# Kernel optimization log

Hardware: AMD Instinct MI355X
Metric: run time of the kernel (lower is better)

## Reference

```python
import jax, jax.numpy as jnp
import numpy as np

N_NODES = 50000
N_EDGES = 800000
F_EXP = 128
F_CNV = 64
HID = 128
N_CLASSES = 10
N_GRAPHS = 64
SLOPE = 0.2


def setup_inputs() -> dict:
    key = jax.random.key(0)
    ks = jax.random.split(key, 24)
    inp = {
        "exp": jax.random.normal(ks[0], (N_NODES, F_EXP), dtype=jnp.float32),
        "cnv": jax.random.normal(ks[1], (N_NODES, F_CNV), dtype=jnp.float32),
        "edge_index": jax.random.randint(ks[2], (2, N_EDGES), 0, N_NODES, dtype=jnp.int64 if jax.config.jax_enable_x64 else jnp.int32),
        "batch": jnp.sort(jax.random.randint(ks[3], (N_NODES,), 0, N_GRAPHS)),
    }
    s = 0.02
    def lin(k, fi, fo):
        kw, kb = jax.random.split(k)
        return (jax.random.normal(kw, (fi, fo), jnp.float32) * s,
                jax.random.normal(kb, (fo,), jnp.float32) * s)
    inp["eps1e"] = jnp.zeros((), jnp.float32)
    inp["W1e"], inp["b1e"] = lin(ks[4], F_EXP, HID)
    inp["eps2e"] = jnp.zeros((), jnp.float32)
    inp["W2e"], inp["b2e"] = lin(ks[5], HID, HID)
    inp["eps1c"] = jnp.zeros((), jnp.float32)
    inp["W1c"], inp["b1c"] = lin(ks[6], F_CNV, HID)
    inp["eps2c"] = jnp.zeros((), jnp.float32)
    inp["W2c"], inp["b2c"] = lin(ks[7], HID, HID)
    inp["Wm"], inp["bm"] = lin(ks[8], 2 * HID, HID)
    inp["Wp1"], inp["bp1"] = lin(ks[9], HID, HID)
    inp["Wp2"], inp["bp2"] = lin(ks[10], HID, N_CLASSES)
    return inp


def _lrelu(x):
    return jnp.where(x > 0, x, SLOPE * x)


def _forward(exp, cnv, src, dst, batch,
             eps1e, W1e, b1e, eps2e, W2e, b2e,
             eps1c, W1c, b1c, eps2c, W2c, b2c,
             Wm, bm, Wp1, bp1, Wp2, bp2):
    N = exp.shape[0]

    def gin(x, eps, W, b):
        # scatter-add neighbor aggregation over edges (self-loops included in src/dst)
        agg = jax.ops.segment_sum(x[src], dst, num_segments=N)
        return ((1.0 + eps) * x + agg) @ W + b

    x_exp = _lrelu(gin(exp, eps1e, W1e, b1e))
    x_exp = _lrelu(gin(x_exp, eps2e, W2e, b2e))
    x_cnv = _lrelu(gin(cnv, eps1c, W1c, b1c))
    x_cnv = _lrelu(gin(x_cnv, eps2c, W2c, b2c))
    x = jnp.concatenate([x_exp, x_cnv], axis=1) @ Wm + bm
    x = _lrelu(x)

    # global mean pool over graph ids
    counts = jax.ops.segment_sum(jnp.ones((N,), x.dtype), batch, num_segments=N_GRAPHS)
    counts = jnp.maximum(counts, 1.0)[:, None]
    graph_repr = jax.ops.segment_sum(x, batch, num_segments=N_GRAPHS) / counts

    logits_nodes = _lrelu(x @ Wp1 + bp1)  # nn.ReLU in mlp -> actually ReLU
    logits_nodes = jnp.maximum(x @ Wp1 + bp1, 0.0) @ Wp2 + bp2
    graph_logits = jax.ops.segment_sum(logits_nodes, batch, num_segments=N_GRAPHS) / counts
    return graph_repr, graph_logits


def reference(exp, cnv, edge_index, batch,
              eps1e, W1e, b1e, eps2e, W2e, b2e,
              eps1c, W1c, b1c, eps2c, W2c, b2c,
              Wm, bm, Wp1, bp1, Wp2, bp2):
    N = exp.shape[0]
    loop = jnp.arange(N, dtype=edge_index.dtype)
    src = jnp.concatenate([edge_index[0], loop])
    dst = jnp.concatenate([edge_index[1], loop])
    return _forward(exp, cnv, src, dst, batch,
                    eps1e, W1e, b1e, eps2e, W2e, b2e,
                    eps1c, W1c, b1c, eps2c, W2c, b2c,
                    Wm, bm, Wp1, bp1, Wp2, bp2)
```

## Files before the change

### kernel.cpp

```cpp
#include <hip/hip_runtime.h>

#define N_NODES 50000
#define N_PAD   50016
#define N_EDGES 800000
#define HID 128
#define NCLS 10
#define NG 64
#define PWAVE 32
#define NB_SCAN ((N_NODES + 255) / 256)

#define EPART 8
#define PRANGE ((N_NODES + EPART - 1) / EPART)
#define ECHUNK 4096
#define NCHUNK ((N_EDGES + ECHUNK - 1) / ECHUNK)

typedef unsigned int uint32;
typedef __attribute__((ext_vector_type(8))) short bf16x8;
typedef __attribute__((ext_vector_type(4))) float f32x4;

__device__ __forceinline__ unsigned short f2bf(float f) {
    uint32 u = __float_as_uint(f);
    uint32 r = u + 0x7fffu + ((u >> 16) & 1u);
    return (unsigned short)(r >> 16);
}
__device__ __forceinline__ float bflo(uint32 v) { return __uint_as_float(v << 16); }
__device__ __forceinline__ float bfhi(uint32 v) { return __uint_as_float(v & 0xffff0000u); }
__device__ __forceinline__ uint32 packbf(float a, float b) {
    return (uint32)f2bf(a) | ((uint32)f2bf(b) << 16);
}


__global__ __launch_bounds__(256) void count_part_k(const int* __restrict__ dst,
                                                    int* __restrict__ deg) {
    int part = blockIdx.x & 7;
    int chunk = blockIdx.x >> 3;
    int lo = part * PRANGE;
    int hi = min(lo + PRANGE, N_NODES);
    int e0 = chunk * ECHUNK;
    int e1 = min(e0 + ECHUNK, N_EDGES);
    for (int i = e0 + threadIdx.x; i < e1; i += 256) {
        int d = dst[i];
        if (d >= lo && d < hi) atomicAdd(&deg[d], 1);
    }
}

__global__ __launch_bounds__(256) void scatter_part_k(const int* __restrict__ src,
                                                      const int* __restrict__ dst,
                                                      int* __restrict__ cursor,
                                                      int* __restrict__ csr) {
    int part = blockIdx.x & 7;
    int chunk = blockIdx.x >> 3;
    int lo = part * PRANGE;
    int hi = min(lo + PRANGE, N_NODES);
    int e0 = chunk * ECHUNK;
    int e1 = min(e0 + ECHUNK, N_EDGES);
    for (int i = e0 + threadIdx.x; i < e1; i += 256) {
        int d = dst[i];
        if (d >= lo && d < hi) {
            int pos = atomicAdd(&cursor[d], 1);
            csr[pos] = src[i];
        }
    }
}

__global__ void gbounds_k(const int* __restrict__ batch, int* __restrict__ gstart) {
    int i = blockIdx.x * blockDim.x + threadIdx.x;
    if (i >= N_NODES) return;
    int b = batch[i];
    int prev = (i == 0) ? -1 : batch[i - 1];
    for (int g = prev + 1; g <= b; g++) gstart[g] = i;
    if (i == N_NODES - 1) {
        for (int g = b + 1; g <= NG; g++) gstart[g] = N_NODES;
    }
}

__device__ __forceinline__ int block_excl_scan_256(int v, int tid, int* total_out) {
    int lane = tid & 63, w = tid >> 6;
    int x = v;
#pragma unroll
    for (int off = 1; off < 64; off <<= 1) {
        int y = __shfl_up(x, off, 64);
        if (lane >= off) x += y;
    }
    __shared__ int wsum[4];
    if (lane == 63) wsum[w] = x;
    __syncthreads();
    int add = 0;
#pragma unroll
    for (int i = 0; i < 4; i++) add += (i < w) ? wsum[i] : 0;
    int total = wsum[0] + wsum[1] + wsum[2] + wsum[3];
    if (total_out) *total_out = total;
    return x - v + add;
}

__global__ __launch_bounds__(256) void scan_partial_k(const int* __restrict__ deg,
                                                      int* __restrict__ rowptr,
                                                      int* __restrict__ blocksum) {
    int tid = threadIdx.x;
    int gid = blockIdx.x * 256 + tid;
    int v = (gid < N_NODES) ? deg[gid] : 0;
    int total;
    int excl = block_excl_scan_256(v, tid, &total);
    if (gid < N_NODES) rowptr[gid] = excl;
    if (tid == 0) blocksum[blockIdx.x] = total;
}

__global__ __launch_bounds__(256) void scan_root_k(const int* __restrict__ blocksum,
                                                   int* __restrict__ blockoff,
                                                   const int* __restrict__ gstart,
                                                   float* __restrict__ invcnt) {
    int tid = threadIdx.x;
    int v = (tid < NB_SCAN) ? blocksum[tid] : 0;
    int excl = block_excl_scan_256(v, tid, nullptr);
    if (tid < NB_SCAN) blockoff[tid] = excl;
    if (tid < NG) {
        int c = gstart[tid + 1] - gstart[tid];
        invcnt[tid] = (c > 0) ? 1.0f / (float)c : 0.0f;
    }
}

__global__ __launch_bounds__(256) void scan_add_k(int* __restrict__ rowptr,
                                                  int* __restrict__ cursor,
                                                  const int* __restrict__ blockoff) {
    int gid = blockIdx.x * 256 + threadIdx.x;
    if (gid < N_NODES) {
        int r = rowptr[gid] + blockoff[blockIdx.x];
        rowptr[gid] = r;
        cursor[gid] = r;
    }
    if (gid == 0) rowptr[N_NODES] = N_EDGES;
}


__global__ __launch_bounds__(256) void conv_both_k(const float* __restrict__ inE,
                                                   unsigned short* __restrict__ outE, int n4e,
                                                   const float* __restrict__ inC,
                                                   unsigned short* __restrict__ outC, int n4c) {
    int i = blockIdx.x * 256 + threadIdx.x;
    const float* in;
    unsigned short* out;
    if (i < n4e) { in = inE; out = outE; }
    else { i -= n4e; if (i >= n4c) return; in = inC; out = outC; }
    float4 v = *(const float4*)(in + (size_t)i * 4);
    uint2 o = {packbf(v.x, v.y), packbf(v.z, v.w)};
    *(uint2*)(out + (size_t)i * 4) = o;
}

__global__ __launch_bounds__(256) void wconv_all_k(const float* W1e, const float* W2e,
                                                   const float* W1c, const float* W2c,
                                                   const float* Wm, const float* Wp1,
                                                   unsigned short* WT1e, unsigned short* WT2e,
                                                   unsigned short* WT1c, unsigned short* WT2c,
                                                   unsigned short* WTm1, unsigned short* WTm2,
                                                   unsigned short* WTp1) {
    int b = blockIdx.x;
    int t = threadIdx.x;
    const float* W; unsigned short* WT; int i; int K;
    if (b < 64)       { W = W1e; WT = WT1e; i = b * 256 + t;          K = 128; }
    else if (b < 128) { W = W2e; WT = WT2e; i = (b - 64) * 256 + t;   K = 128; }
    else if (b < 160) { W = W1c; WT = WT1c; i = (b - 128) * 256 + t;  K = 64;  }
    else if (b < 224) { W = W2c; WT = WT2c; i = (b - 160) * 256 + t;  K = 128; }
    else if (b < 352) {
        i = (b - 224) * 256 + t;
        int k = i >> 7, n = i & 127;
        unsigned short v = f2bf(Wm[i]);
        if (k < 128) WTm1[n * 128 + k] = v;
        else         WTm2[n * 128 + (k - 128)] = v;
        return;
    }
    else              { W = Wp1; WT = WTp1; i = (b - 352) * 256 + t;  K = 128; }
    int k = i >> 7, n = i & 127;
    if (k < K) WT[n * K + k] = f2bf(W[i]);
}


__device__ __forceinline__ uint32 agg_row128(const uint32* __restrict__ X,
                                             const int* __restrict__ rowptr,
                                             const int* __restrict__ csr,
                                             int n, int lane, float scale) {
    uint32 xv = X[(size_t)n * 64 + lane];
    float a0 = scale * bflo(xv);
    float a1 = scale * bfhi(xv);
    int e = rowptr[n], e1 = rowptr[n + 1];
    for (; e + 8 <= e1; e += 8) {
        int i0 = csr[e],     i1 = csr[e + 1], i2 = csr[e + 2], i3 = csr[e + 3];
        int i4 = csr[e + 4], i5 = csr[e + 5], i6 = csr[e + 6], i7 = csr[e + 7];
        uint32 v0 = X[(size_t)i0 * 64 + lane];
        uint32 v1 = X[(size_t)i1 * 64 + lane];
        uint32 v2 = X[(size_t)i2 * 64 + lane];
        uint32 v3 = X[(size_t)i3 * 64 + lane];
        uint32 v4 = X[(size_t)i4 * 64 + lane];
        uint32 v5 = X[(size_t)i5 * 64 + lane];
        uint32 v6 = X[(size_t)i6 * 64 + lane];
        uint32 v7 = X[(size_t)i7 * 64 + lane];
        a0 += bflo(v0) + bflo(v1) + bflo(v2) + bflo(v3) +
              bflo(v4) + bflo(v5) + bflo(v6) + bflo(v7);
        a1 += bfhi(v0) + bfhi(v1) + bfhi(v2) + bfhi(v3) +
              bfhi(v4) + bfhi(v5) + bfhi(v6) + bfhi(v7);
    }
    if (e + 4 <= e1) {
        int i0 = csr[e], i1 = csr[e + 1], i2 = csr[e + 2], i3 = csr[e + 3];
        uint32 v0 = X[(size_t)i0 * 64 + lane];
        uint32 v1 = X[(size_t)i1 * 64 + lane];
        uint32 v2 = X[(size_t)i2 * 64 + lane];
        uint32 v3 = X[(size_t)i3 * 64 + lane];
        a0 += bflo(v0) + bflo(v1) + bflo(v2) + bflo(v3);
        a1 += bfhi(v0) + bfhi(v1) + bfhi(v2) + bfhi(v3);
        e += 4;
    }
    for (; e < e1; e++) {
        uint32 v = X[(size_t)csr[e] * 64 + lane];
        a0 += bflo(v);
        a1 += bfhi(v);
    }
    return packbf(a0, a1);
}


__global__ __launch_bounds__(256) void agg_gemm_k(const uint32* __restrict__ X1,
                                                  const float* __restrict__ eps1,
                                                  const unsigned short* __restrict__ WT1p,
                                                  const float* __restrict__ b1,
                                                  unsigned short* __restrict__ out1,
                                                  const uint32* __restrict__ X2,
                                                  const float* __restrict__ eps2,
                                                  const unsigned short* __restrict__ WT2p,
                                                  const float* __restrict__ b2,
                                                  unsigned short* __restrict__ out2,
                                                  const int* __restrict__ rowptr,
                                                  const int* __restrict__ csr,
                                                  int nblk1) {
    __shared__ uint32 lds[32 * 64];
    int blk = blockIdx.x;
    const uint32* X; const float* epsp; const unsigned short* WT;
    const float* bias; unsigned short* out;
    if (blk < nblk1) { X = X1; epsp = eps1; WT = WT1p; bias = b1; out = out1; }
    else { blk -= nblk1; X = X2; epsp = eps2; WT = WT2p; bias = b2; out = out2; }

    int tid = threadIdx.x;
    int w = tid >> 6, lane = tid & 63;
    int base = blk * 32;
    float scale = 2.0f + epsp[0];

    for (int s = 0; s < 8; s++) {
        int lrow = w * 8 + s;
        int n = base + lrow;
        uint32 outv = 0;
        if (n < N_NODES) outv = agg_row128(X, rowptr, csr, n, lane, scale);
        int byte = (lrow * 256 + lane * 4) ^ ((lrow & 7) << 4);
        lds[byte >> 2] = outv;
    }
    __syncthreads();

    int m = lane & 15, g = lane >> 4;
    int lrow = (w & 1) * 16 + m;
    int row16 = base + (w & 1) * 16;
    int col16 = (w >> 1) * 64;

    f32x4 acc[4];
#pragma unroll
    for (int nt = 0; nt < 4; nt++) acc[nt] = (f32x4){0.f, 0.f, 0.f, 0.f};

    const unsigned short* bp = WT + (size_t)(col16 + m) * 128 + g * 8;
#pragma unroll
    for (int k0 = 0; k0 < 128; k0 += 32) {
        int ab = (lrow * 256 + (g * 8 + k0) * 2) ^ ((lrow & 7) << 4);
        bf16x8 af = *(const bf16x8*)((const char*)lds + ab);
#pragma unroll
        for (int nt = 0; nt < 4; nt++) {
            bf16x8 bfv = *(const bf16x8*)(bp + (size_t)nt * 16 * 128 + k0);
            acc[nt] = __builtin_amdgcn_mfma_f32_16x16x32_bf16(af, bfv, acc[nt], 0, 0, 0);
        }
    }

#pragma unroll
    for (int nt = 0; nt < 4; nt++) {
        int col = col16 + nt * 16 + m;
        float bv = bias[col];
#pragma unroll
        for (int r = 0; r < 4; r++) {
            int row = row16 + g * 4 + r;
            if (row < N_NODES) {
                float v = acc[nt][r] + bv;
                v = v > 0.f ? v : 0.2f * v;
                out[(size_t)row * 128 + col] = f2bf(v);
            }
        }
    }
}


__global__ __launch_bounds__(256) void agg64_bf_k(const uint32* __restrict__ X,
                                                  const int* __restrict__ rowptr,
                                                  const int* __restrict__ csr,
                                                  const float* __restrict__ eps,
                                                  uint32* __restrict__ H) {
    int hw = (blockIdx.x * 256 + threadIdx.x) >> 5;
    int lane = threadIdx.x & 31;
    if (hw >= N_NODES) return;
    float scale = 2.0f + eps[0];
    uint32 xv = X[(size_t)hw * 32 + lane];
    float a0 = scale * bflo(xv);
    float a1 = scale * bfhi(xv);
    int e = rowptr[hw], e1 = rowptr[hw + 1];
    for (; e + 8 <= e1; e += 8) {
        int i0 = csr[e],     i1 = csr[e + 1], i2 = csr[e + 2], i3 = csr[e + 3];
        int i4 = csr[e + 4], i5 = csr[e + 5], i6 = csr[e + 6], i7 = csr[e + 7];
        uint32 v0 = X[(size_t)i0 * 32 + lane];
        uint32 v1 = X[(size_t)i1 * 32 + lane];
        uint32 v2 = X[(size_t)i2 * 32 + lane];
        uint32 v3 = X[(size_t)i3 * 32 + lane];
        uint32 v4 = X[(size_t)i4 * 32 + lane];
        uint32 v5 = X[(size_t)i5 * 32 + lane];
        uint32 v6 = X[(size_t)i6 * 32 + lane];
        uint32 v7 = X[(size_t)i7 * 32 + lane];
        a0 += bflo(v0) + bflo(v1) + bflo(v2) + bflo(v3) +
              bflo(v4) + bflo(v5) + bflo(v6) + bflo(v7);
        a1 += bfhi(v0) + bfhi(v1) + bfhi(v2) + bfhi(v3) +
              bfhi(v4) + bfhi(v5) + bfhi(v6) + bfhi(v7);
    }
    if (e + 4 <= e1) {
        int i0 = csr[e], i1 = csr[e + 1], i2 = csr[e + 2], i3 = csr[e + 3];
        uint32 v0 = X[(size_t)i0 * 32 + lane];
        uint32 v1 = X[(size_t)i1 * 32 + lane];
        uint32 v2 = X[(size_t)i2 * 32 + lane];
        uint32 v3 = X[(size_t)i3 * 32 + lane];
        a0 += bflo(v0) + bflo(v1) + bflo(v2) + bflo(v3);
        a1 += bfhi(v0) + bfhi(v1) + bfhi(v2) + bfhi(v3);
        e += 4;
    }
    for (; e < e1; e++) {
        uint32 v = X[(size_t)csr[e] * 32 + lane];
        a0 += bflo(v);
        a1 += bfhi(v);
    }
    H[(size_t)hw * 32 + lane] = packbf(a0, a1);
}


__global__ __launch_bounds__(256) void gemm_bf_k(const unsigned short* __restrict__ A1,
                                                 const unsigned short* __restrict__ WT1, int K1,
                                                 const unsigned short* __restrict__ A2,
                                                 const unsigned short* __restrict__ WT2, int K2,
                                                 const float* __restrict__ bias,
                                                 unsigned short* __restrict__ out, int act) {
    int tid = threadIdx.x;
    int w = tid >> 6, l = tid & 63;
    int row16 = blockIdx.x * 32 + (w & 1) * 16;
    int col16 = (w >> 1) * 64;
    int m = l & 15, g = l >> 4;

    f32x4 acc[4];
#pragma unroll
    for (int nt = 0; nt < 4; nt++) acc[nt] = (f32x4){0.f, 0.f, 0.f, 0.f};

    const unsigned short* A = A1;
    const unsigned short* WT = WT1;
    int K = K1;
    for (int pass = 0; pass < 2; ++pass) {
        if (pass) {
            if (A2 == nullptr) break;
            A = A2; WT = WT2; K = K2;
        }
        const unsigned short* ap = A + (size_t)(row16 + m) * K + g * 8;
        const unsigned short* bp = WT + (size_t)(col16 + m) * K + g * 8;
        for (int k0 = 0; k0 < K; k0 += 32) {
            bf16x8 af = *(const bf16x8*)(ap + k0);
#pragma unroll
            for (int nt = 0; nt < 4; nt++) {
                bf16x8 bfv = *(const bf16x8*)(bp + (size_t)nt * 16 * K + k0);
                acc[nt] = __builtin_amdgcn_mfma_f32_16x16x32_bf16(af, bfv, acc[nt], 0, 0, 0);
            }
        }
    }

#pragma unroll
    for (int nt = 0; nt < 4; nt++) {
        int col = col16 + nt * 16 + m;
        float bv = bias[col];
#pragma unroll
        for (int r = 0; r < 4; r++) {
            int row = row16 + g * 4 + r;
            if (row < N_NODES) {
                float v = acc[nt][r] + bv;
                if (act == 1) v = v > 0.f ? v : 0.2f * v;
                else if (act == 2) v = fmaxf(v, 0.f);
                out[(size_t)row * 128 + col] = f2bf(v);
            }
        }
    }
}


__global__ __launch_bounds__(256) void pool2_bf_k(const uint32* __restrict__ D,
                                                  const uint32* __restrict__ T,
                                                  const int* __restrict__ batch,
                                                  float* __restrict__ sumD,
                                                  float* __restrict__ sumT) {
    int wv = (blockIdx.x * 256 + threadIdx.x) >> 6;
    int f = threadIdx.x & 63;
    int i0 = wv * PWAVE;
    if (i0 >= N_NODES) return;
    int i1 = min(i0 + PWAVE, N_NODES);
    float d0 = 0.f, d1 = 0.f, t0 = 0.f, t1 = 0.f;
    int g = batch[i0];
    int i = i0;
    for (; i + 4 <= i1; i += 4) {
        int b0 = batch[i], b1 = batch[i + 1], b2 = batch[i + 2], b3 = batch[i + 3];
        uint32 dv0 = D[(size_t)i * 64 + f];
        uint32 dv1 = D[(size_t)(i + 1) * 64 + f];
        uint32 dv2 = D[(size_t)(i + 2) * 64 + f];
        uint32 dv3 = D[(size_t)(i + 3) * 64 + f];
        uint32 tv0 = T[(size_t)i * 64 + f];
        uint32 tv1 = T[(size_t)(i + 1) * 64 + f];
        uint32 tv2 = T[(size_t)(i + 2) * 64 + f];
        uint32 tv3 = T[(size_t)(i + 3) * 64 + f];
#define POOL_STEP(bg, dv, tv)                                          \
        if (bg != g) {                                                 \
            atomicAdd(&sumD[g * 128 + 2 * f], d0);                     \
            atomicAdd(&sumD[g * 128 + 2 * f + 1], d1);                 \
            atomicAdd(&sumT[g * 128 + 2 * f], t0);                     \
            atomicAdd(&sumT[g * 128 + 2 * f + 1], t1);                 \
            d0 = d1 = t0 = t1 = 0.f; g = bg;                           \
        }                                                              \
        d0 += bflo(dv); d1 += bfhi(dv);                                \
        t0 += bflo(tv); t1 += bfhi(tv);
        POOL_STEP(b0, dv0, tv0)
        POOL_STEP(b1, dv1, tv1)
        POOL_STEP(b2, dv2, tv2)
        POOL_STEP(b3, dv3, tv3)
    }
    for (; i < i1; i++) {
        int bg = batch[i];
        uint32 dv = D[(size_t)i * 64 + f];
        uint32 tv = T[(size_t)i * 64 + f];
        POOL_STEP(bg, dv, tv)
    }
#undef POOL_STEP
    atomicAdd(&sumD[g * 128 + 2 * f], d0);
    atomicAdd(&sumD[g * 128 + 2 * f + 1], d1);
    atomicAdd(&sumT[g * 128 + 2 * f], t0);
    atomicAdd(&sumT[g * 128 + 2 * f + 1], t1);
}


__global__ __launch_bounds__(128) void finalize_k(const float* __restrict__ sumD,
                                                  const float* __restrict__ sumT,
                                                  const float* __restrict__ invcnt,
                                                  const float* __restrict__ Wp2,
                                                  const float* __restrict__ bp2,
                                                  float* __restrict__ out) {
    __shared__ float tr[128];
    int g = blockIdx.x;
    int f = threadIdx.x;
    float ic = invcnt[g];
    out[g * 128 + f] = sumD[g * 128 + f] * ic;
    tr[f] = sumT[g * 128 + f] * ic;
    __syncthreads();
    if (f < NCLS) {
        float acc = (ic > 0.f) ? bp2[f] : 0.f;
        for (int k = 0; k < 128; k++) acc = fmaf(tr[k], Wp2[k * NCLS + f], acc);
        out[NG * 128 + g * NCLS + f] = acc;
    }
}


extern "C" void kernel_launch(void* const* d_in, const int* in_sizes, int n_in,
                              void* d_out, int out_size, void* d_ws, size_t ws_size,
                              hipStream_t stream) {
    const float* exp_f = (const float*)d_in[0];
    const float* cnv_f = (const float*)d_in[1];
    const int*   ei    = (const int*)d_in[2];
    const int*   batch = (const int*)d_in[3];
    const float* eps1e = (const float*)d_in[4];
    const float* W1e   = (const float*)d_in[5];
    const float* b1e   = (const float*)d_in[6];
    const float* eps2e = (const float*)d_in[7];
    const float* W2e   = (const float*)d_in[8];
    const float* b2e   = (const float*)d_in[9];
    const float* eps1c = (const float*)d_in[10];
    const float* W1c   = (const float*)d_in[11];
    const float* b1c   = (const float*)d_in[12];
    const float* eps2c = (const float*)d_in[13];
    const float* W2c   = (const float*)d_in[14];
    const float* b2c   = (const float*)d_in[15];
    const float* Wm    = (const float*)d_in[16];
    const float* bm    = (const float*)d_in[17];
    const float* Wp1   = (const float*)d_in[18];
    const float* bp1   = (const float*)d_in[19];
    const float* Wp2   = (const float*)d_in[20];
    const float* bp2   = (const float*)d_in[21];
    float* out = (float*)d_out;

    char* ws = (char*)d_ws;
    size_t off = 0;
    auto alloc = [&](size_t bytes) -> void* {
        void* p = ws + off;
        off = (off + bytes + 255) & ~(size_t)255;
        return p;
    };
    int* deg      = (int*)alloc((size_t)N_NODES * 4);
    int* rowptr   = (int*)alloc((size_t)(N_NODES + 1) * 4);
    int* cursor   = (int*)alloc((size_t)N_NODES * 4);
    int* csr      = (int*)alloc((size_t)N_EDGES * 4);
    int* gstart   = (int*)alloc((NG + 1) * 4);
    float* invcnt = (float*)alloc(NG * 4);
    int* blocksum = (int*)alloc(NB_SCAN * 4);
    int* blockoff = (int*)alloc(NB_SCAN * 4);
    float* sumD   = (float*)alloc((size_t)NG * 128 * 4);
    float* sumT   = (float*)alloc((size_t)NG * 128 * 4);

    unsigned short* Xe = (unsigned short*)alloc((size_t)N_PAD * 128 * 2);
    unsigned short* Xc = (unsigned short*)alloc((size_t)N_PAD * 64 * 2);
    unsigned short* E  = (unsigned short*)alloc((size_t)N_PAD * 64 * 2);
    unsigned short* B  = (unsigned short*)alloc((size_t)N_PAD * 128 * 2);
    unsigned short* C  = (unsigned short*)alloc((size_t)N_PAD * 128 * 2);
    unsigned short* B2 = (unsigned short*)alloc((size_t)N_PAD * 128 * 2);
    unsigned short* C2 = (unsigned short*)alloc((size_t)N_PAD * 128 * 2);
    unsigned short* D  = (unsigned short*)alloc((size_t)N_PAD * 128 * 2);
    unsigned short* T  = (unsigned short*)alloc((size_t)N_PAD * 128 * 2);

    unsigned short* WT1e = (unsigned short*)alloc(128 * 128 * 2);
    unsigned short* WT2e = (unsigned short*)alloc(128 * 128 * 2);
    unsigned short* WT1c = (unsigned short*)alloc(128 * 64 * 2);
    unsigned short* WT2c = (unsigned short*)alloc(128 * 128 * 2);
    unsigned short* WTm1 = (unsigned short*)alloc(128 * 128 * 2);
    unsigned short* WTm2 = (unsigned short*)alloc(128 * 128 * 2);
    unsigned short* WTp1 = (unsigned short*)alloc(128 * 128 * 2);

    const int* src = ei;
    const int* dst = ei + N_EDGES;

    hipMemsetAsync(deg, 0, (size_t)N_NODES * 4, stream);
    hipMemsetAsync(sumD, 0, (size_t)NG * 128 * 4 * 2, stream);

    count_part_k<<<NCHUNK * EPART, 256, 0, stream>>>(dst, deg);
    gbounds_k<<<(N_NODES + 255) / 256, 256, 0, stream>>>(batch, gstart);
    scan_partial_k<<<NB_SCAN, 256, 0, stream>>>(deg, rowptr, blocksum);
    scan_root_k<<<1, 256, 0, stream>>>(blocksum, blockoff, gstart, invcnt);
    scan_add_k<<<NB_SCAN, 256, 0, stream>>>(rowptr, cursor, blockoff);
    scatter_part_k<<<NCHUNK * EPART, 256, 0, stream>>>(src, dst, cursor, csr);

    const int n4e = N_NODES * 128 / 4, n4c = N_NODES * 64 / 4;
    conv_both_k<<<(n4e + n4c + 255) / 256, 256, 0, stream>>>(exp_f, Xe, n4e, cnv_f, Xc, n4c);
    wconv_all_k<<<416, 256, 0, stream>>>(W1e, W2e, W1c, W2c, Wm, Wp1,
                                         WT1e, WT2e, WT1c, WT2c, WTm1, WTm2, WTp1);

    const int AGG64_GRID = (N_NODES * 32 + 255) / 256;
    const int GEMM_GRID = (N_NODES + 31) / 32;

    agg_gemm_k<<<GEMM_GRID, 256, 0, stream>>>((const uint32*)Xe, eps1e, WT1e, b1e, B,
                                              nullptr, nullptr, nullptr, nullptr, nullptr,
                                              rowptr, csr, GEMM_GRID);
    agg64_bf_k<<<AGG64_GRID, 256, 0, stream>>>((const uint32*)Xc, rowptr, csr, eps1c, (uint32*)E);
    gemm_bf_k<<<GEMM_GRID, 256, 0, stream>>>(E, WT1c, 64, nullptr, nullptr, 0, b1c, C, 1);
    agg_gemm_k<<<2 * GEMM_GRID, 256, 0, stream>>>((const uint32*)B, eps2e, WT2e, b2e, B2,
                                                  (const uint32*)C, eps2c, WT2c, b2c, C2,
                                                  rowptr, csr, GEMM_GRID);
    gemm_bf_k<<<GEMM_GRID, 256, 0, stream>>>(B2, WTm1, 128, C2, WTm2, 128, bm, D, 1);
    gemm_bf_k<<<GEMM_GRID, 256, 0, stream>>>(D, WTp1, 128, nullptr, nullptr, 0, bp1, T, 2);
    const int POOL_GRID = ((N_NODES + PWAVE - 1) / PWAVE * 64 + 255) / 256;
    pool2_bf_k<<<POOL_GRID, 256, 0, stream>>>((const uint32*)D, (const uint32*)T,
                                              batch, sumD, sumT);
    finalize_k<<<NG, 128, 0, stream>>>(sumD, sumT, invcnt, Wp2, bp2, out);
}
```

Baseline: 452.4 us.

## Fuse preprocessing kernels and merge 64-wide conv aggregation into combined agg-GEMM launch

```diff
diff --git a/kernel.cpp b/kernel.cpp
--- a/kernel.cpp
+++ b/kernel.cpp
@@ -27,6 +27,83 @@
 __device__ __forceinline__ float bfhi(uint32 v) { return __uint_as_float(v & 0xffff0000u); }
 __device__ __forceinline__ uint32 packbf(float a, float b) {
     return (uint32)f2bf(a) | ((uint32)f2bf(b) << 16);
+}
+
+
+#define PRE_N4E (N_NODES * 128 / 4)
+#define PRE_N4C (N_NODES * 64 / 4)
+#define PRE_CB ((PRE_N4E + PRE_N4C + 255) / 256)
+#define PRE_ZB ((N_NODES + 255) / 256)
+#define PRE_TOTAL (PRE_CB + PRE_ZB + 1 + PRE_ZB + 416)
+
+__global__ __launch_bounds__(256) void pre_k(const float* __restrict__ exp_f,
+                                             unsigned short* __restrict__ Xe,
+                                             const float* __restrict__ cnv_f,
+                                             unsigned short* __restrict__ Xc,
+                                             int* __restrict__ deg,
+                                             float* __restrict__ sums,
+                                             const int* __restrict__ batch,
+                                             int* __restrict__ gstart,
+                                             const float* W1e, const float* W2e,
+                                             const float* W1c, const float* W2c,
+                                             const float* Wm, const float* Wp1,
+                                             unsigned short* WT1e, unsigned short* WT2e,
+                                             unsigned short* WT1c, unsigned short* WT2c,
+                                             unsigned short* WTm1, unsigned short* WTm2,
+                                             unsigned short* WTp1) {
+    int b = blockIdx.x;
+    int t = threadIdx.x;
+    if (b < PRE_CB) {
+        int i = b * 256 + t;
+        const float* in;
+        unsigned short* out;
+        if (i < PRE_N4E) { in = exp_f; out = Xe; }
+        else { i -= PRE_N4E; if (i >= PRE_N4C) return; in = cnv_f; out = Xc; }
+        float4 v = *(const float4*)(in + (size_t)i * 4);
+        uint2 o = {packbf(v.x, v.y), packbf(v.z, v.w)};
+        *(uint2*)(out + (size_t)i * 4) = o;
+        return;
+    }
+    b -= PRE_CB;
+    if (b < PRE_ZB) {
+        int i = b * 256 + t;
+        if (i < N_NODES) deg[i] = 0;
+        return;
+    }
+    b -= PRE_ZB;
+    if (b == 0) {
+        for (int i = t; i < 2 * NG * 128; i += 256) sums[i] = 0.f;
+        return;
+    }
+    b -= 1;
+    if (b < PRE_ZB) {
+        int i = b * 256 + t;
+        if (i >= N_NODES) return;
+        int bb = batch[i];
+        int prev = (i == 0) ? -1 : batch[i - 1];
+        for (int g = prev + 1; g <= bb; g++) gstart[g] = i;
+        if (i == N_NODES - 1) {
+            for (int g = bb + 1; g <= NG; g++) gstart[g] = N_NODES;
+        }
+        return;
+    }
+    b -= PRE_ZB;
+    const float* W; unsigned short* WT; int i; int K;
+    if (b < 64)       { W = W1e; WT = WT1e; i = b * 256 + t;          K = 128; }
+    else if (b < 128) { W = W2e; WT = WT2e; i = (b - 64) * 256 + t;   K = 128; }
+    else if (b < 160) { W = W1c; WT = WT1c; i = (b - 128) * 256 + t;  K = 64;  }
+    else if (b < 224) { W = W2c; WT = WT2c; i = (b - 160) * 256 + t;  K = 128; }
+    else if (b < 352) {
+        i = (b - 224) * 256 + t;
+        int k = i >> 7, n = i & 127;
+        unsigned short v = f2bf(Wm[i]);
+        if (k < 128) WTm1[n * 128 + k] = v;
+        else         WTm2[n * 128 + (k - 128)] = v;
+        return;
+    }
+    else              { W = Wp1; WT = WTp1; i = (b - 352) * 256 + t;  K = 128; }
+    int k = i >> 7, n = i & 127;
+    if (k < K) WT[n * K + k] = f2bf(W[i]);
 }
 
 
@@ -63,17 +140,6 @@
     }
 }
 
-__global__ void gbounds_k(const int* __restrict__ batch, int* __restrict__ gstart) {
-    int i = blockIdx.x * blockDim.x + threadIdx.x;
-    if (i >= N_NODES) return;
-    int b = batch[i];
-    int prev = (i == 0) ? -1 : batch[i - 1];
-    for (int g = prev + 1; g <= b; g++) gstart[g] = i;
-    if (i == N_NODES - 1) {
-        for (int g = b + 1; g <= NG; g++) gstart[g] = N_NODES;
-    }
-}
-
 __device__ __forceinline__ int block_excl_scan_256(int v, int tid, int* total_out) {
     int lane = tid & 63, w = tid >> 6;
     int x = v;
@@ -132,48 +198,6 @@
 }
 
 
-__global__ __launch_bounds__(256) void conv_both_k(const float* __restrict__ inE,
-                                                   unsigned short* __restrict__ outE, int n4e,
-                                                   const float* __restrict__ inC,
-                                                   unsigned short* __restrict__ outC, int n4c) {
-    int i = blockIdx.x * 256 + threadIdx.x;
-    const float* in;
-    unsigned short* out;
-    if (i < n4e) { in = inE; out = outE; }
-    else { i -= n4e; if (i >= n4c) return; in = inC; out = outC; }
-    float4 v = *(const float4*)(in + (size_t)i * 4);
-    uint2 o = {packbf(v.x, v.y), packbf(v.z, v.w)};
-    *(uint2*)(out + (size_t)i * 4) = o;
-}
-
-__global__ __launch_bounds__(256) void wconv_all_k(const float* W1e, const float* W2e,
-                                                   const float* W1c, const float* W2c,
-                                                   const float* Wm, const float* Wp1,
-                                                   unsigned short* WT1e, unsigned short* WT2e,
-                                                   unsigned short* WT1c, unsigned short* WT2c,
-                                                   unsigned short* WTm1, unsigned short* WTm2,
-                                                   unsigned short* WTp1) {
-    int b = blockIdx.x;
-    int t = threadIdx.x;
-    const float* W; unsigned short* WT; int i; int K;
-    if (b < 64)       { W = W1e; WT = WT1e; i = b * 256 + t;          K = 128; }
-    else if (b < 128) { W = W2e; WT = WT2e; i = (b - 64) * 256 + t;   K = 128; }
-    else if (b < 160) { W = W1c; WT = WT1c; i = (b - 128) * 256 + t;  K = 64;  }
-    else if (b < 224) { W = W2c; WT = WT2c; i = (b - 160) * 256 + t;  K = 128; }
-    else if (b < 352) {
-        i = (b - 224) * 256 + t;
-        int k = i >> 7, n = i & 127;
-        unsigned short v = f2bf(Wm[i]);
-        if (k < 128) WTm1[n * 128 + k] = v;
-        else         WTm2[n * 128 + (k - 128)] = v;
-        return;
-    }
-    else              { W = Wp1; WT = WTp1; i = (b - 352) * 256 + t;  K = 128; }
-    int k = i >> 7, n = i & 127;
-    if (k < K) WT[n * K + k] = f2bf(W[i]);
-}
-
-
 __device__ __forceinline__ uint32 agg_row128(const uint32* __restrict__ X,
                                              const int* __restrict__ rowptr,
                                              const int* __restrict__ csr,
@@ -182,34 +206,72 @@
     float a0 = scale * bflo(xv);
     float a1 = scale * bfhi(xv);
     int e = rowptr[n], e1 = rowptr[n + 1];
-    for (; e + 8 <= e1; e += 8) {
-        int i0 = csr[e],     i1 = csr[e + 1], i2 = csr[e + 2], i3 = csr[e + 3];
-        int i4 = csr[e + 4], i5 = csr[e + 5], i6 = csr[e + 6], i7 = csr[e + 7];
-        uint32 v0 = X[(size_t)i0 * 64 + lane];
-        uint32 v1 = X[(size_t)i1 * 64 + lane];
-        uint32 v2 = X[(size_t)i2 * 64 + lane];
-        uint32 v3 = X[(size_t)i3 * 64 + lane];
-        uint32 v4 = X[(size_t)i4 * 64 + lane];
-        uint32 v5 = X[(size_t)i5 * 64 + lane];
-        uint32 v6 = X[(size_t)i6 * 64 + lane];
-        uint32 v7 = X[(size_t)i7 * 64 + lane];
-        a0 += bflo(v0) + bflo(v1) + bflo(v2) + bflo(v3) +
-              bflo(v4) + bflo(v5) + bflo(v6) + bflo(v7);
-        a1 += bfhi(v0) + bfhi(v1) + bfhi(v2) + bfhi(v3) +
-              bfhi(v4) + bfhi(v5) + bfhi(v6) + bfhi(v7);
+    for (; e + 16 <= e1; e += 16) {
+        int idx[16]; uint32 vv[16];
+#pragma unroll
+        for (int j = 0; j < 16; j++) idx[j] = csr[e + j];
+#pragma unroll
+        for (int j = 0; j < 16; j++) vv[j] = X[(size_t)idx[j] * 64 + lane];
+#pragma unroll
+        for (int j = 0; j < 16; j++) { a0 += bflo(vv[j]); a1 += bfhi(vv[j]); }
+    }
+    if (e + 8 <= e1) {
+        int idx[8]; uint32 vv[8];
+#pragma unroll
+        for (int j = 0; j < 8; j++) idx[j] = csr[e + j];
+#pragma unroll
+        for (int j = 0; j < 8; j++) vv[j] = X[(size_t)idx[j] * 64 + lane];
+#pragma unroll
+        for (int j = 0; j < 8; j++) { a0 += bflo(vv[j]); a1 += bfhi(vv[j]); }
+        e += 8;
     }
     if (e + 4 <= e1) {
-        int i0 = csr[e], i1 = csr[e + 1], i2 = csr[e + 2], i3 = csr[e + 3];
-        uint32 v0 = X[(size_t)i0 * 64 + lane];
-        uint32 v1 = X[(size_t)i1 * 64 + lane];
-        uint32 v2 = X[(size_t)i2 * 64 + lane];
-        uint32 v3 = X[(size_t)i3 * 64 + lane];
-        a0 += bflo(v0) + bflo(v1) + bflo(v2) + bflo(v3);
-        a1 += bfhi(v0) + bfhi(v1) + bfhi(v2) + bfhi(v3);
+        int idx[4]; uint32 vv[4];
+#pragma unroll
+        for (int j = 0; j < 4; j++) idx[j] = csr[e + j];
+#pragma unroll
+        for (int j = 0; j < 4; j++) vv[j] = X[(size_t)idx[j] * 64 + lane];
+#pragma unroll
+        for (int j = 0; j < 4; j++) { a0 += bflo(vv[j]); a1 += bfhi(vv[j]); }
         e += 4;
     }
     for (; e < e1; e++) {
         uint32 v = X[(size_t)csr[e] * 64 + lane];
+        a0 += bflo(v);
+        a1 += bfhi(v);
+    }
+    return packbf(a0, a1);
+}
+
+__device__ __forceinline__ uint32 agg_row64(const uint32* __restrict__ X,
+                                            const int* __restrict__ rowptr,
+                                            const int* __restrict__ csr,
+                                            int n, int lane32, float scale) {
+    uint32 xv = X[(size_t)n * 32 + lane32];
+    float a0 = scale * bflo(xv);
+    float a1 = scale * bfhi(xv);
+    int e = rowptr[n], e1 = rowptr[n + 1];
+    for (; e + 8 <= e1; e += 8) {
+        int idx[8]; uint32 vv[8];
+#pragma unroll
+        for (int j = 0; j < 8; j++) idx[j] = csr[e + j];
+#pragma unroll
+        for (int j = 0; j < 8; j++) vv[j] = X[(size_t)idx[j] * 32 + lane32];
+#pragma unroll
+        for (int j = 0; j < 8; j++) { a0 += bflo(vv[j]); a1 += bfhi(vv[j]); }
+    }
+    if (e + 4 <= e1) {
+        int idx[4]; uint32 vv[4];
+#pragma unroll
+        for (int j = 0; j < 4; j++) idx[j] = csr[e + j];
+#pragma unroll
+        for (int j = 0; j < 4; j++) vv[j] = X[(size_t)idx[j] * 32 + lane32];
+#pragma unroll
+        for (int j = 0; j < 4; j++) { a0 += bflo(vv[j]); a1 += bfhi(vv[j]); }
+        e += 4;
+    }
+    for (; e < e1; e++) {
+        uint32 v = X[(size_t)csr[e] * 32 + lane32];
         a0 += bflo(v);
         a1 += bfhi(v);
     }
@@ -229,26 +291,42 @@
                                                   unsigned short* __restrict__ out2,
                                                   const int* __restrict__ rowptr,
                                                   const int* __restrict__ csr,
-                                                  int nblk1) {
+                                                  int nblk1, int K2) {
     __shared__ uint32 lds[32 * 64];
     int blk = blockIdx.x;
-    const uint32* X; const float* epsp; const unsigned short* WT;
-    const float* bias; unsigned short* out;
-    if (blk < nblk1) { X = X1; epsp = eps1; WT = WT1p; bias = b1; out = out1; }
-    else { blk -= nblk1; X = X2; epsp = eps2; WT = WT2p; bias = b2; out = out2; }
+    bool second = blk >= nblk1;
+    if (second) blk -= nblk1;
+    const uint32* X = second ? X2 : X1;
+    const float* epsp = second ? eps2 : eps1;
+    const unsigned short* WT = second ? WT2p : WT1p;
+    const float* bias = second ? b2 : b1;
+    unsigned short* out = second ? out2 : out1;
+    int K = second ? K2 : 128;
 
     int tid = threadIdx.x;
     int w = tid >> 6, lane = tid & 63;
     int base = blk * 32;
     float scale = 2.0f + epsp[0];
 
-    for (int s = 0; s < 8; s++) {
-        int lrow = w * 8 + s;
-        int n = base + lrow;
-        uint32 outv = 0;
-        if (n < N_NODES) outv = agg_row128(X, rowptr, csr, n, lane, scale);
-        int byte = (lrow * 256 + lane * 4) ^ ((lrow & 7) << 4);
-        lds[byte >> 2] = outv;
+    if (K == 128) {
+        for (int s = 0; s < 8; s++) {
+            int lrow = w * 8 + s;
+            int n = base + lrow;
+            uint32 outv = 0;
+            if (n < N_NODES) outv = agg_row128(X, rowptr, csr, n, lane, scale);
+            int byte = (lrow * 256 + lane * 4) ^ ((lrow & 7) << 4);
+            lds[byte >> 2] = outv;
+        }
+    } else {
+        int half = lane >> 5, lane32 = lane & 31;
+        for (int s = 0; s < 4; s++) {
+            int lrow = w * 8 + 2 * s + half;
+            int n = base + lrow;
+            uint32 outv = 0;
+            if (n < N_NODES) outv = agg_row64(X, rowptr, csr, n, lane32, scale);
+            int byte = (lrow * 128 + lane32 * 4) ^ ((lrow & 7) << 4);
+            lds[byte >> 2] = outv;
+        }
     }
     __syncthreads();
 
@@ -261,14 +339,14 @@
 #pragma unroll
     for (int nt = 0; nt < 4; nt++) acc[nt] = (f32x4){0.f, 0.f, 0.f, 0.f};
 
-    const unsigned short* bp = WT + (size_t)(col16 + m) * 128 + g * 8;
-#pragma unroll
-    for (int k0 = 0; k0 < 128; k0 += 32) {
-        int ab = (lrow * 256 + (g * 8 + k0) * 2) ^ ((lrow & 7) << 4);
+    const unsigned short* bp = WT + (size_t)(col16 + m) * K + g * 8;
+    int rowbytes = K * 2;
+    for (int k0 = 0; k0 < K; k0 += 32) {
+        int ab = (lrow * rowbytes + (g * 8 + k0) * 2) ^ ((lrow & 7) << 4);
         bf16x8 af = *(const bf16x8*)((const char*)lds + ab);
 #pragma unroll
         for (int nt = 0; nt < 4; nt++) {
-            bf16x8 bfv = *(const bf16x8*)(bp + (size_t)nt * 16 * 128 + k0);
+            bf16x8 bfv = *(const bf16x8*)(bp + (size_t)nt * 16 * K + k0);
             acc[nt] = __builtin_amdgcn_mfma_f32_16x16x32_bf16(af, bfv, acc[nt], 0, 0, 0);
         }
     }
@@ -287,54 +365,6 @@
             }
         }
     }
-}
-
-
-__global__ __launch_bounds__(256) void agg64_bf_k(const uint32* __restrict__ X,
-                                                  const int* __restrict__ rowptr,
-                                                  const int* __restrict__ csr,
-                                                  const float* __restrict__ eps,
-                                                  uint32* __restrict__ H) {
-    int hw = (blockIdx.x * 256 + threadIdx.x) >> 5;
-    int lane = threadIdx.x & 31;
-    if (hw >= N_NODES) return;
-    float scale = 2.0f + eps[0];
-    uint32 xv = X[(size_t)hw * 32 + lane];
-    float a0 = scale * bflo(xv);
-    float a1 = scale * bfhi(xv);
-    int e = rowptr[hw], e1 = rowptr[hw + 1];
-    for (; e + 8 <= e1; e += 8) {
-        int i0 = csr[e],     i1 = csr[e + 1], i2 = csr[e + 2], i3 = csr[e + 3];
-        int i4 = csr[e + 4], i5 = csr[e + 5], i6 = csr[e + 6], i7 = csr[e + 7];
-        uint32 v0 = X[(size_t)i0 * 32 + lane];
-        uint32 v1 = X[(size_t)i1 * 32 + lane];
-        uint32 v2 = X[(size_t)i2 * 32 + lane];
-        uint32 v3 = X[(size_t)i3 * 32 + lane];
-        uint32 v4 = X[(size_t)i4 * 32 + lane];
-        uint32 v5 = X[(size_t)i5 * 32 + lane];
-        uint32 v6 = X[(size_t)i6 * 32 + lane];
-        uint32 v7 = X[(size_t)i7 * 32 + lane];
-        a0 += bflo(v0) + bflo(v1) + bflo(v2) + bflo(v3) +
-              bflo(v4) + bflo(v5) + bflo(v6) + bflo(v7);
-        a1 += bfhi(v0) + bfhi(v1) + bfhi(v2) + bfhi(v3) +
-              bfhi(v4) + bfhi(v5) + bfhi(v6) + bfhi(v7);
-    }
-    if (e + 4 <= e1) {
-        int i0 = csr[e], i1 = csr[e + 1], i2 = csr[e + 2], i3 = csr[e + 3];
-        uint32 v0 = X[(size_t)i0 * 32 + lane];
-        uint32 v1 = X[(size_t)i1 * 32 + lane];
-        uint32 v2 = X[(size_t)i2 * 32 + lane];
-        uint32 v3 = X[(size_t)i3 * 32 + lane];
-        a0 += bflo(v0) + bflo(v1) + bflo(v2) + bflo(v3);
-        a1 += bfhi(v0) + bfhi(v1) + bfhi(v2) + bfhi(v3);
-        e += 4;
-    }
-    for (; e < e1; e++) {
-        uint32 v = X[(size_t)csr[e] * 32 + lane];
-        a0 += bflo(v);
-        a1 += bfhi(v);
-    }
-    H[(size_t)hw * 32 + lane] = packbf(a0, a1);
 }
 
 
@@ -512,7 +542,6 @@
 
     unsigned short* Xe = (unsigned short*)alloc((size_t)N_PAD * 128 * 2);
     unsigned short* Xc = (unsigned short*)alloc((size_t)N_PAD * 64 * 2);
-    unsigned short* E  = (unsigned short*)alloc((size_t)N_PAD * 64 * 2);
     unsigned short* B  = (unsigned short*)alloc((size_t)N_PAD * 128 * 2);
     unsigned short* C  = (unsigned short*)alloc((size_t)N_PAD * 128 * 2);
     unsigned short* B2 = (unsigned short*)alloc((size_t)N_PAD * 128 * 2);
@@ -531,32 +560,23 @@
     const int* src = ei;
     const int* dst = ei + N_EDGES;
 
-    hipMemsetAsync(deg, 0, (size_t)N_NODES * 4, stream);
-    hipMemsetAsync(sumD, 0, (size_t)NG * 128 * 4 * 2, stream);
-
+    pre_k<<<PRE_TOTAL, 256, 0, stream>>>(exp_f, Xe, cnv_f, Xc, deg, sumD, batch, gstart,
+                                         W1e, W2e, W1c, W2c, Wm, Wp1,
+                                         WT1e, WT2e, WT1c, WT2c, WTm1, WTm2, WTp1);
     count_part_k<<<NCHUNK * EPART, 256, 0, stream>>>(dst, deg);
-    gbounds_k<<<(N_NODES + 255) / 256, 256, 0, stream>>>(batch, gstart);
     scan_partial_k<<<NB_SCAN, 256, 0, stream>>>(deg, rowptr, blocksum);
     scan_root_k<<<1, 256, 0, stream>>>(blocksum, blockoff, gstart, invcnt);
     scan_add_k<<<NB_SCAN, 256, 0, stream>>>(rowptr, cursor, blockoff);
     scatter_part_k<<<NCHUNK * EPART, 256, 0, stream>>>(src, dst, cursor, csr);
 
-    const int n4e = N_NODES * 128 / 4, n4c = N_NODES * 64 / 4;
-    conv_both_k<<<(n4e + n4c + 255) / 256, 256, 0, stream>>>(exp_f, Xe, n4e, cnv_f, Xc, n4c);
-    wconv_all_k<<<416, 256, 0, stream>>>(W1e, W2e, W1c, W2c, Wm, Wp1,
-                                         WT1e, WT2e, WT1c, WT2c, WTm1, WTm2, WTp1);
-
-    const int AGG64_GRID = (N_NODES * 32 + 255) / 256;
     const int GEMM_GRID = (N_NODES + 31) / 32;
 
-    agg_gemm_k<<<GEMM_GRID, 256, 0, stream>>>((const uint32*)Xe, eps1e, WT1e, b1e, B,
-                                              nullptr, nullptr, nullptr, nullptr, nullptr,
-                                              rowptr, csr, GEMM_GRID);
-    agg64_bf_k<<<AGG64_GRID, 256, 0, stream>>>((const uint32*)Xc, rowptr, csr, eps1c, (uint32*)E);
-    gemm_bf_k<<<GEMM_GRID, 256, 0, stream>>>(E, WT1c, 64, nullptr, nullptr, 0, b1c, C, 1);
+    agg_gemm_k<<<2 * GEMM_GRID, 256, 0, stream>>>((const uint32*)Xe, eps1e, WT1e, b1e, B,
+                                                  (const uint32*)Xc, eps1c, WT1c, b1c, C,
+                                                  rowptr, csr, GEMM_GRID, 64);
     agg_gemm_k<<<2 * GEMM_GRID, 256, 0, stream>>>((const uint32*)B, eps2e, WT2e, b2e, B2,
                                                   (const uint32*)C, eps2c, WT2c, b2c, C2,
-                                                  rowptr, csr, GEMM_GRID);
+                                                  rowptr, csr, GEMM_GRID, 128);
     gemm_bf_k<<<GEMM_GRID, 256, 0, stream>>>(B2, WTm1, 128, C2, WTm2, 128, bm, D, 1);
     gemm_bf_k<<<GEMM_GRID, 256, 0, stream>>>(D, WTp1, 128, nullptr, nullptr, 0, bp1, T, 2);
     const int POOL_GRID = ((N_NODES + PWAVE - 1) / PWAVE * 64 + 255) / 256;
```

Result: no change. 458.0 us (+1.2%).
